# Kernel tuning notes

Hardware: AMD Instinct MI355X
Metric: run time of the kernel (lower is better)

## Reference

```python
import jax, jax.numpy as jnp
import numpy as np

B, S, H, NH = 4, 2048, 1024, 16
D = H // NH

def setup_inputs() -> dict:
    key = jax.random.key(0)
    ks = jax.random.split(key, 9)
    sc = 1.0 / np.sqrt(H)
    return {
        "x": jax.random.normal(ks[0], (B, S, H), jnp.float32),
        "Wq": jax.random.normal(ks[1], (H, H), jnp.float32) * sc,
        "bq": jax.random.normal(ks[2], (H,), jnp.float32) * 0.01,
        "Wk": jax.random.normal(ks[3], (H, H), jnp.float32) * sc,
        "bk": jax.random.normal(ks[4], (H,), jnp.float32) * 0.01,
        "Wv": jax.random.normal(ks[5], (H, H), jnp.float32) * sc,
        "bv": jax.random.normal(ks[6], (H,), jnp.float32) * 0.01,
        "Wo": jax.random.normal(ks[7], (H, H), jnp.float32) * sc,
        "bo": jax.random.normal(ks[8], (H,), jnp.float32) * 0.01,
    }

def reference(x, Wq, bq, Wk, bk, Wv, bv, Wo, bo):
    # torch Linear: y = x @ W.T + b
    def proj(x, W, b):
        # [B,S,H] -> [B,NH,S,D]
        y = jnp.einsum('bsh,oh->bso', x, W) + b
        return y.reshape(B, S, NH, D).transpose(0, 2, 1, 3)
    q = proj(x, Wq, bq)
    k = proj(x, Wk, bk)
    v = proj(x, Wv, bv)
    scores = jnp.einsum('bhqd,bhkd->bhqk', q, k) / jnp.sqrt(jnp.float32(D))
    p = jax.nn.softmax(scores, axis=-1)  # [B,NH,S,S]
    o = jnp.einsum('bhqk,bhkd->bhqd', p, v)  # dropout p=0 (eval)
    o = o.transpose(0, 2, 1, 3).reshape(B, S, H)
    return jnp.einsum('bsh,oh->bso', o, Wo) + bo
```

## Files before the change

kernel.cpp:

```cpp
#include <hip/hip_runtime.h>


#define DEV __device__ __forceinline__

typedef __bf16 bf16x8 __attribute__((ext_vector_type(8)));
typedef __bf16 bf16x4 __attribute__((ext_vector_type(4)));
typedef __bf16 bf16x2 __attribute__((ext_vector_type(2)));
typedef float floatx4 __attribute__((ext_vector_type(4)));
typedef unsigned int uintx4 __attribute__((ext_vector_type(4)));

constexpr int Bdim = 4, SS = 2048, HH = 1024, NHH = 16, DD = 64;
constexpr int MM = Bdim * SS;

DEV void async16(const void* g, void* l) {
  __builtin_amdgcn_global_load_lds(
      (const __attribute__((address_space(1))) unsigned int*)g,
      (__attribute__((address_space(3))) unsigned int*)l, 16, 0, 0);
}

DEV int swz3(int r) { return (r ^ (r >> 3)) & 7; }

DEV unsigned pkbf16(float lo, float hi) {
  bf16x2 t;
  t[0] = (__bf16)lo;
  t[1] = (__bf16)hi;
  return __builtin_bit_cast(unsigned, t);
}

DEV void pswap16(unsigned& a, unsigned& b) {
  asm("v_permlane16_swap_b32 %0, %1" : "+v"(a), "+v"(b));
}

__global__ __launch_bounds__(256) void cast_bf16_kernel(
    const float* __restrict__ x, const float* __restrict__ wq,
    const float* __restrict__ wk, const float* __restrict__ wv,
    const float* __restrict__ wo,
    __bf16* __restrict__ xb, __bf16* __restrict__ wqb, __bf16* __restrict__ wkb,
    __bf16* __restrict__ wvb, __bf16* __restrict__ wob) {
  const float* src; __bf16* dst; int n4;
  switch (blockIdx.z) {
    case 0: src = x;  dst = xb;  n4 = MM * HH / 4; break;
    case 1: src = wq; dst = wqb; n4 = HH * HH / 4; break;
    case 2: src = wk; dst = wkb; n4 = HH * HH / 4; break;
    case 3: src = wv; dst = wvb; n4 = HH * HH / 4; break;
    default: src = wo; dst = wob; n4 = HH * HH / 4; break;
  }
  int stride = gridDim.x * blockDim.x;
  for (int i = blockIdx.x * blockDim.x + threadIdx.x; i < n4; i += stride) {
    float4 v = ((const float4*)src)[i];
    bf16x4 o;
    o[0] = (__bf16)v.x; o[1] = (__bf16)v.y; o[2] = (__bf16)v.z; o[3] = (__bf16)v.w;
    ((bf16x4*)dst)[i] = o;
  }
}

DEV void gemm8p(const __bf16* __restrict__ Ablk, const __bf16* __restrict__ Bblk,
                __bf16* Ab, __bf16* Bb, floatx4 acc[4][4]) {
  const int t = threadIdx.x;
  const int lane = t & 63, quad = lane >> 4, l16 = lane & 15;
  const int wid = t >> 6;
  const int wm = (wid >> 2) * 64, wn = (wid & 3) * 64;

  const int rl = t >> 3, ch = t & 7;
  const __bf16* Ag[2];
  Ag[0] = Ablk + (size_t)rl * HH + (ch ^ swz3(rl)) * 8;
  Ag[1] = Ablk + (size_t)(rl + 64) * HH + (ch ^ swz3(rl + 64)) * 8;
  const __bf16* Bg[4];
#pragma unroll
  for (int br = 0; br < 4; ++br)
    Bg[br] = Bblk + (size_t)(rl + 64 * br) * HH + (ch ^ swz3(rl + 64 * br)) * 8;

  int aoff[2][4], boff[2][4];
#pragma unroll
  for (int kk = 0; kk < 2; ++kk)
#pragma unroll
    for (int i = 0; i < 4; ++i) {
      int ra = wm + i * 16 + l16;
      aoff[kk][i] = ra * 64 + (((kk * 4 + quad) ^ swz3(ra)) * 8);
      int rb = wn + i * 16 + l16;
      boff[kk][i] = rb * 64 + (((kk * 4 + quad) ^ swz3(rb)) * 8);
    }

#pragma unroll
  for (int tile = 0; tile < 2; ++tile) {
    async16(Ag[0] + tile * 64, Ab + tile * 8192 + t * 8);
    async16(Ag[1] + tile * 64, Ab + tile * 8192 + 4096 + t * 8);
#pragma unroll
    for (int br = 0; br < 4; ++br)
      async16(Bg[br] + tile * 64, Bb + tile * 16384 + br * 4096 + t * 8);
  }
  asm volatile("s_waitcnt vmcnt(6)" ::: "memory");
  __builtin_amdgcn_s_barrier();

  int cb = 0, sb = 2;
#pragma unroll 1
  for (int kt = 0; kt < 16; ++kt) {
    const __bf16* Ac = Ab + cb * 8192;
    const __bf16* Bc = Bb + cb * 16384;
    __bf16* Asg = Ab + sb * 8192;
    __bf16* Bsg = Bb + sb * 16384;
    const int ks = (kt + 2) * 64;
    const bool st = kt < 14;

    bf16x8 af[4], bfr[4];
#pragma unroll
    for (int i = 0; i < 4; ++i) af[i] = *(const bf16x8*)&Ac[aoff[0][i]];
#pragma unroll
    for (int i = 0; i < 4; ++i) bfr[i] = *(const bf16x8*)&Bc[boff[0][i]];
    if (st) {
      async16(Ag[0] + ks, Asg + t * 8);
      async16(Ag[1] + ks, Asg + 4096 + t * 8);
      async16(Bg[0] + ks, Bsg + t * 8);
    }
    asm volatile("" ::: "memory");
    __builtin_amdgcn_s_barrier();
    asm volatile("s_waitcnt lgkmcnt(0)" ::: "memory");
    __builtin_amdgcn_sched_barrier(0);
    __builtin_amdgcn_s_setprio(1);
#pragma unroll
    for (int mi = 0; mi < 4; ++mi)
#pragma unroll
      for (int ni = 0; ni < 4; ++ni)
        acc[mi][ni] = __builtin_amdgcn_mfma_f32_16x16x32_bf16(af[mi], bfr[ni],
                                                              acc[mi][ni], 0, 0, 0);
    __builtin_amdgcn_s_setprio(0);
    asm volatile("" ::: "memory");
    __builtin_amdgcn_s_barrier();

#pragma unroll
    for (int i = 0; i < 4; ++i) af[i] = *(const bf16x8*)&Ac[aoff[1][i]];
#pragma unroll
    for (int i = 0; i < 4; ++i) bfr[i] = *(const bf16x8*)&Bc[boff[1][i]];
    if (st) {
      async16(Bg[1] + ks, Bsg + 4096 + t * 8);
      async16(Bg[2] + ks, Bsg + 8192 + t * 8);
      async16(Bg[3] + ks, Bsg + 12288 + t * 8);
    }
    asm volatile("" ::: "memory");
    __builtin_amdgcn_s_barrier();
    asm volatile("s_waitcnt lgkmcnt(0)" ::: "memory");
    __builtin_amdgcn_sched_barrier(0);
    __builtin_amdgcn_s_setprio(1);
#pragma unroll
    for (int mi = 0; mi < 4; ++mi)
#pragma unroll
      for (int ni = 0; ni < 4; ++ni)
        acc[mi][ni] = __builtin_amdgcn_mfma_f32_16x16x32_bf16(af[mi], bfr[ni],
                                                              acc[mi][ni], 0, 0, 0);
    __builtin_amdgcn_s_setprio(0);
    if (st) asm volatile("s_waitcnt vmcnt(6)" ::: "memory");
    else    asm volatile("s_waitcnt vmcnt(0)" ::: "memory");
    asm volatile("" ::: "memory");
    __builtin_amdgcn_s_barrier();

    cb = cb == 2 ? 0 : cb + 1;
    sb = sb == 2 ? 0 : sb + 1;
  }
}

__global__ __launch_bounds__(512, 2) void proj_qkv_kernel(
    const __bf16* __restrict__ xb,
    const __bf16* __restrict__ wqb, const __bf16* __restrict__ wkb,
    const __bf16* __restrict__ wvb,
    const float* __restrict__ bq, const float* __restrict__ bk,
    const float* __restrict__ bv,
    __bf16* __restrict__ Q, __bf16* __restrict__ Kc, __bf16* __restrict__ Vt) {
  __shared__ __align__(16) __bf16 Ab[3][128 * 64];
  __shared__ __align__(16) __bf16 Bb[3][256 * 64];

  const int lid = blockIdx.x;
  const int xcd = lid & 7, slot = lid >> 3;
  const int mp = xcd + 8 * (slot & 7);
  const int nt = slot >> 3;
  const int mode = nt >> 2;
  const int n0 = (nt & 3) * 256;
  const int m0 = mp * 128;

  const __bf16* W = mode == 0 ? wqb : mode == 1 ? wkb : wvb;
  const float* bias = mode == 0 ? bq : mode == 1 ? bk : bv;

  floatx4 acc[4][4] = {};
  gemm8p(xb + (size_t)m0 * HH, W + (size_t)n0 * HH, &Ab[0][0], &Bb[0][0], acc);

  const int t = threadIdx.x, lane = t & 63, quad = lane >> 4, l16 = lane & 15;
  const int wid = t >> 6, wm = (wid >> 2) * 64, wn = (wid & 3) * 64;
  const float qscale = 0.125f * 1.44269504088896f;

#pragma unroll
  for (int ni = 0; ni < 4; ++ni) {
    int n = n0 + wn + ni * 16 + l16;
    float bval = bias[n];
    int h = n >> 6, d = n & 63;
#pragma unroll
    for (int mi = 0; mi < 4; ++mi) {
      int mbase = m0 + wm + mi * 16 + quad * 4;
      int bb = mbase >> 11, sbase = mbase & (SS - 1);
      size_t bh = (size_t)(bb * NHH + h);
      if (mode == 2) {
        bf16x4 pv;
#pragma unroll
        for (int r = 0; r < 4; ++r) pv[r] = (__bf16)(acc[mi][ni][r] + bval);
        *(bf16x4*)&Vt[(bh * DD + d) * SS + sbase] = pv;
      } else {
#pragma unroll
        for (int r = 0; r < 4; ++r) {
          float v = acc[mi][ni][r] + bval;
          if (mode == 0) Q [(bh * SS + sbase + r) * DD + d] = (__bf16)(v * qscale);
          else           Kc[(bh * SS + sbase + r) * DD + d] = (__bf16)v;
        }
      }
    }
  }
}

__global__ __launch_bounds__(512, 2) void proj_out_kernel(
    const __bf16* __restrict__ Ob, const __bf16* __restrict__ wob,
    const float* __restrict__ bo, float* __restrict__ out) {
  __shared__ __align__(16) __bf16 Ab[3][128 * 64];
  __shared__ __align__(16) __bf16 Bb[3][256 * 64];

  const int lid = blockIdx.x;
  const int xcd = lid & 7, slot = lid >> 3;
  const int mp = xcd + 8 * (slot & 7);
  const int np = slot >> 3;
  const int m0 = mp * 128, n0 = np * 256;

  floatx4 acc[4][4] = {};
  gemm8p(Ob + (size_t)m0 * HH, wob + (size_t)n0 * HH, &Ab[0][0], &Bb[0][0], acc);

  const int t = threadIdx.x, lane = t & 63, quad = lane >> 4, l16 = lane & 15;
  const int wid = t >> 6, wm = (wid >> 2) * 64, wn = (wid & 3) * 64;
#pragma unroll
  for (int ni = 0; ni < 4; ++ni) {
    int n = n0 + wn + ni * 16 + l16;
    float bval = bo[n];
#pragma unroll
    for (int mi = 0; mi < 4; ++mi)
#pragma unroll
      for (int r = 0; r < 4; ++r) {
        int m = m0 + wm + mi * 16 + quad * 4 + r;
        out[(size_t)m * HH + n] = acc[mi][ni][r] + bval;
      }
  }
}

__global__ __launch_bounds__(256, 2) void attn_kernel(
    const __bf16* __restrict__ Q, const __bf16* __restrict__ Kc,
    const __bf16* __restrict__ Vt, __bf16* __restrict__ Ob) {
  __shared__ __align__(16) __bf16 Ks[2][64 * 64];
  __shared__ __align__(16) __bf16 Vs[2][64 * 64];

  const int t = threadIdx.x, lane = t & 63, quad = lane >> 4, l16 = lane & 15;
  const int wid = t >> 6;
  const int L = blockIdx.x;
  const int qt = L >> 6, bhx = L & 63;
  const int b = bhx >> 4, h = bhx & 15;
  const size_t bh = (size_t)b * NHH + h;
  const __bf16* Qg = Q + (bh * SS + (size_t)qt * 256) * DD;
  const __bf16* Kg = Kc + bh * SS * DD;
  const __bf16* Vg = Vt + bh * DD * SS;

  const int srow = t >> 3;
  const int sc = t & 7;

  const __bf16* KgA = Kg + (size_t)srow * DD + (sc ^ swz3(srow)) * 8;
  const __bf16* KgB = Kg + (size_t)(srow + 32) * DD + (sc ^ swz3(srow + 32)) * 8;
  const __bf16* VgA = Vg + (size_t)srow * SS + (sc ^ swz3(srow)) * 8;
  const __bf16* VgB = Vg + (size_t)(srow + 32) * SS + (sc ^ swz3(srow + 32)) * 8;

  bf16x8 qf[4][2];
#pragma unroll
  for (int ni = 0; ni < 4; ++ni)
#pragma unroll
    for (int ks = 0; ks < 2; ++ks)
      qf[ni][ks] = *(const bf16x8*)(Qg + (size_t)(wid * 64 + ni * 16 + l16) * DD
                                    + (ks * 4 + quad) * 8);

  floatx4 oacc[4][4] = {};
  float rsum[4] = {0.f, 0.f, 0.f, 0.f};

  int koff[4][2];
#pragma unroll
  for (int mi = 0; mi < 4; ++mi) {
    int r = mi * 16 + l16;
#pragma unroll
    for (int ks = 0; ks < 2; ++ks)
      koff[mi][ks] = r * 64 + ((ks * 4 + quad) ^ swz3(r)) * 8;
  }
  const int sq = ((quad & 1) << 1) | (quad >> 1);
  int voff[4][2];
#pragma unroll
  for (int nj = 0; nj < 4; ++nj) {
    int r = nj * 16 + l16;
#pragma unroll
    for (int hf = 0; hf < 2; ++hf)
      voff[nj][hf] = r * 64 + ((hf * 4 + sq) ^ swz3(r)) * 8;
  }

  async16(KgA, &Ks[0][t * 8]);
  async16(KgB, &Ks[0][2048 + t * 8]);
  async16(VgA, &Vs[0][t * 8]);
  async16(VgB, &Vs[0][2048 + t * 8]);

  for (int kt = 0; kt < SS / 64; ++kt) {
    const int cur = kt & 1;
    __syncthreads();

    if (kt + 1 < SS / 64) {
      const int kk = (kt + 1) * 64;
      const int nxt = cur ^ 1;
      async16(KgA + (size_t)kk * DD, &Ks[nxt][t * 8]);
      async16(KgB + (size_t)kk * DD, &Ks[nxt][2048 + t * 8]);
      async16(VgA + kk, &Vs[nxt][t * 8]);
      async16(VgB + kk, &Vs[nxt][2048 + t * 8]);
    }

    floatx4 sacc[4][4];
#pragma unroll
    for (int mi = 0; mi < 4; ++mi)
#pragma unroll
      for (int ni = 0; ni < 4; ++ni) sacc[mi][ni] = floatx4{0.f, 0.f, 0.f, 0.f};
#pragma unroll
    for (int ks = 0; ks < 2; ++ks) {
      bf16x8 kf[4];
#pragma unroll
      for (int mi = 0; mi < 4; ++mi) kf[mi] = *(const bf16x8*)&Ks[cur][koff[mi][ks]];
#pragma unroll
      for (int mi = 0; mi < 4; ++mi)
#pragma unroll
        for (int ni = 0; ni < 4; ++ni)
          sacc[mi][ni] = __builtin_amdgcn_mfma_f32_16x16x32_bf16(kf[mi], qf[ni][ks],
                                                                 sacc[mi][ni], 0, 0, 0);
    }

#pragma unroll
    for (int hf = 0; hf < 2; ++hf) {
      bf16x8 ap[4], bv8[4];
#pragma unroll
      for (int mq = 0; mq < 4; ++mq) {
        float p[2][4];
#pragma unroll
        for (int m = 0; m < 2; ++m)
#pragma unroll
          for (int r = 0; r < 4; ++r) {
            float e = __builtin_amdgcn_exp2f(sacc[hf * 2 + m][mq][r]);
            rsum[mq] += e;
            p[m][r] = e;
          }
        unsigned x0 = pkbf16(p[0][0], p[0][1]);
        unsigned x1 = pkbf16(p[0][2], p[0][3]);
        unsigned y0 = pkbf16(p[1][0], p[1][1]);
        unsigned y1 = pkbf16(p[1][2], p[1][3]);
        pswap16(x0, y0);
        pswap16(x1, y1);
        uintx4 u = {x0, x1, y0, y1};
        ap[mq] = __builtin_bit_cast(bf16x8, u);
      }
#pragma unroll
      for (int nj = 0; nj < 4; ++nj) bv8[nj] = *(const bf16x8*)&Vs[cur][voff[nj][hf]];
#pragma unroll
      for (int mq = 0; mq < 4; ++mq)
#pragma unroll
        for (int nj = 0; nj < 4; ++nj)
          oacc[mq][nj] = __builtin_amdgcn_mfma_f32_16x16x32_bf16(ap[mq], bv8[nj],
                                                                 oacc[mq][nj], 0, 0, 0);
    }
  }

#pragma unroll
  for (int ni = 0; ni < 4; ++ni) {
    rsum[ni] += __shfl_xor(rsum[ni], 16, 64);
    rsum[ni] += __shfl_xor(rsum[ni], 32, 64);
  }

  const int s0 = qt * 256 + wid * 64;
#pragma unroll
  for (int mq = 0; mq < 4; ++mq) {
#pragma unroll
    for (int r = 0; r < 4; ++r) {
      float inv = 1.f / __shfl(rsum[mq], quad * 4 + r, 64);
      int s = s0 + mq * 16 + quad * 4 + r;
#pragma unroll
      for (int nj = 0; nj < 4; ++nj) {
        int d = nj * 16 + l16;
        Ob[((size_t)b * SS + s) * HH + h * DD + d] = (__bf16)(oacc[mq][nj][r] * inv);
      }
    }
  }
}

extern "C" void kernel_launch(void* const* d_in, const int* in_sizes, int n_in,
                              void* d_out, int out_size, void* d_ws, size_t ws_size,
                              hipStream_t stream) {
  const float* x  = (const float*)d_in[0];
  const float* Wq = (const float*)d_in[1];
  const float* bq = (const float*)d_in[2];
  const float* Wk = (const float*)d_in[3];
  const float* bk = (const float*)d_in[4];
  const float* Wv = (const float*)d_in[5];
  const float* bv = (const float*)d_in[6];
  const float* Wo = (const float*)d_in[7];
  const float* bo = (const float*)d_in[8];
  float* out = (float*)d_out;

  char* ws = (char*)d_ws;
  __bf16* xb  = (__bf16*)(ws);
  __bf16* wqb = (__bf16*)(ws + 16777216);
  __bf16* wkb = (__bf16*)(ws + 18874368);
  __bf16* wvb = (__bf16*)(ws + 20971520);
  __bf16* wob = (__bf16*)(ws + 23068672);
  __bf16* Qb  = (__bf16*)(ws + 25165824);
  __bf16* Kb  = (__bf16*)(ws + 41943040);
  __bf16* Vtb = (__bf16*)(ws + 58720256);
  __bf16* Ob  = (__bf16*)(ws + 75497472);

  cast_bf16_kernel<<<dim3(256, 1, 5), 256, 0, stream>>>(x, Wq, Wk, Wv, Wo,
                                                        xb, wqb, wkb, wvb, wob);
  proj_qkv_kernel<<<dim3(768), 512, 0, stream>>>(xb, wqb, wkb, wvb,
                                                 bq, bk, bv, Qb, Kb, Vtb);
  attn_kernel<<<dim3(512), 256, 0, stream>>>(Qb, Kb, Vtb, Ob);
  proj_out_kernel<<<dim3(256), 512, 0, stream>>>(Ob, wob, bo, out);
}
```

Baseline: 268.5 us.

## Compute softmax row sums with MFMA against ones and drop accumulator zeroing

The attention kernel now gets the softmax denominator by running an extra MFMA that multiplies the packed bf16 probabilities by a ones vector, replacing the per-element VALU adds and the cross-lane shuffle reductions. The first QK MFMA takes a zero accumulator directly, so the explicit zero-initialisation of the score accumulators goes away. The row sums are now taken over bf16-rounded probabilities, which matches what multiplies V, and each inner step costs 4 extra MFMAs per 32. Separately, the GEMM prologue waits for all outstanding loads (vmcnt 0) rather than leaving 6 in flight, which adds some stall at startup.

```diff
diff --git a/kernel.cpp b/kernel.cpp
--- a/kernel.cpp
+++ b/kernel.cpp
@@ -89,7 +89,7 @@
     for (int br = 0; br < 4; ++br)
       async16(Bg[br] + tile * 64, Bb + tile * 16384 + br * 4096 + t * 8);
   }
-  asm volatile("s_waitcnt vmcnt(6)" ::: "memory");
+  asm volatile("s_waitcnt vmcnt(0)" ::: "memory");
   __builtin_amdgcn_s_barrier();
 
   int cb = 0, sb = 2;
@@ -277,7 +277,11 @@
                                     + (ks * 4 + quad) * 8);
 
   floatx4 oacc[4][4] = {};
-  float rsum[4] = {0.f, 0.f, 0.f, 0.f};
+  floatx4 rsacc[4] = {};
+  const floatx4 z4 = {0.f, 0.f, 0.f, 0.f};
+  bf16x8 ones;
+#pragma unroll
+  for (int i = 0; i < 8; ++i) ones[i] = (__bf16)1.0f;
 
   int koff[4][2];
 #pragma unroll
@@ -316,20 +320,23 @@
     }
 
     floatx4 sacc[4][4];
-#pragma unroll
-    for (int mi = 0; mi < 4; ++mi)
-#pragma unroll
-      for (int ni = 0; ni < 4; ++ni) sacc[mi][ni] = floatx4{0.f, 0.f, 0.f, 0.f};
-#pragma unroll
-    for (int ks = 0; ks < 2; ++ks) {
+    {
       bf16x8 kf[4];
 #pragma unroll
-      for (int mi = 0; mi < 4; ++mi) kf[mi] = *(const bf16x8*)&Ks[cur][koff[mi][ks]];
+      for (int mi = 0; mi < 4; ++mi) kf[mi] = *(const bf16x8*)&Ks[cur][koff[mi][0]];
 #pragma unroll
       for (int mi = 0; mi < 4; ++mi)
 #pragma unroll
         for (int ni = 0; ni < 4; ++ni)
-          sacc[mi][ni] = __builtin_amdgcn_mfma_f32_16x16x32_bf16(kf[mi], qf[ni][ks],
+          sacc[mi][ni] = __builtin_amdgcn_mfma_f32_16x16x32_bf16(kf[mi], qf[ni][0],
+                                                                 z4, 0, 0, 0);
+#pragma unroll
+      for (int mi = 0; mi < 4; ++mi) kf[mi] = *(const bf16x8*)&Ks[cur][koff[mi][1]];
+#pragma unroll
+      for (int mi = 0; mi < 4; ++mi)
+#pragma unroll
+        for (int ni = 0; ni < 4; ++ni)
+          sacc[mi][ni] = __builtin_amdgcn_mfma_f32_16x16x32_bf16(kf[mi], qf[ni][1],
                                                                  sacc[mi][ni], 0, 0, 0);
     }
 
@@ -342,11 +349,8 @@
 #pragma unroll
         for (int m = 0; m < 2; ++m)
 #pragma unroll
-          for (int r = 0; r < 4; ++r) {
-            float e = __builtin_amdgcn_exp2f(sacc[hf * 2 + m][mq][r]);
-            rsum[mq] += e;
-            p[m][r] = e;
-          }
+          for (int r = 0; r < 4; ++r)
+            p[m][r] = __builtin_amdgcn_exp2f(sacc[hf * 2 + m][mq][r]);
         unsigned x0 = pkbf16(p[0][0], p[0][1]);
         unsigned x1 = pkbf16(p[0][2], p[0][3]);
         unsigned y0 = pkbf16(p[1][0], p[1][1]);
@@ -359,18 +363,15 @@
 #pragma unroll
       for (int nj = 0; nj < 4; ++nj) bv8[nj] = *(const bf16x8*)&Vs[cur][voff[nj][hf]];
 #pragma unroll
-      for (int mq = 0; mq < 4; ++mq)
+      for (int mq = 0; mq < 4; ++mq) {
 #pragma unroll
         for (int nj = 0; nj < 4; ++nj)
           oacc[mq][nj] = __builtin_amdgcn_mfma_f32_16x16x32_bf16(ap[mq], bv8[nj],
                                                                  oacc[mq][nj], 0, 0, 0);
-    }
-  }
-
-#pragma unroll
-  for (int ni = 0; ni < 4; ++ni) {
-    rsum[ni] += __shfl_xor(rsum[ni], 16, 64);
-    rsum[ni] += __shfl_xor(rsum[ni], 32, 64);
+        rsacc[mq] = __builtin_amdgcn_mfma_f32_16x16x32_bf16(ap[mq], ones,
+                                                            rsacc[mq], 0, 0, 0);
+      }
+    }
   }
 
   const int s0 = qt * 256 + wid * 64;
@@ -378,7 +379,7 @@
   for (int mq = 0; mq < 4; ++mq) {
 #pragma unroll
     for (int r = 0; r < 4; ++r) {
-      float inv = 1.f / __shfl(rsum[mq], quad * 4 + r, 64);
+      float inv = 1.f / rsacc[mq][r];
       int s = s0 + mq * 16 + quad * 4 + r;
 #pragma unroll
       for (int nj = 0; nj < 4; ++nj) {
```

Result: no change. 270.8 us (+0.8%).
